# Kernel optimization log

Measured on AMD Instinct MI355X. Metric: run time of the kernel, lower is better.

Reference implementation:

```python
import jax, jax.numpy as jnp
import numpy as np

TAU = 2.0      # LIF membrane time constant (spikingjelly default-style, decay_input=True)
VTH = 0.5      # v_threshold from init
S = 4          # time_steps
EPS = 1e-5     # BatchNorm eps
ALPHA = 4.0    # surrogate sigmoid alpha (spikingjelly Sigmoid default)

@jax.custom_vjp
def spike(x):
    # Heaviside forward (spikingjelly: x >= 0 -> 1)
    return (x >= 0.0).astype(x.dtype)

def _spike_fwd(x):
    return spike(x), x

def _spike_bwd(x, g):
    sg = jax.nn.sigmoid(ALPHA * x)
    return (g * ALPHA * sg * (1.0 - sg),)

spike.defvjp(_spike_fwd, _spike_bwd)

def bn(y, gamma, beta, mean, var):
    # inference-mode BatchNorm2d over channel axis 1; y: (B, C, T, V)
    inv = gamma * jax.lax.rsqrt(var + EPS)
    return y * inv[None, :, None, None] + (beta - mean * inv)[None, :, None, None]


def setup_inputs() -> dict:
    key = jax.random.key(0)
    ks = jax.random.split(key, 16)
    B, T, C, V, H, NC = 16, 512, 3, 16, 128, 12
    inp = {
        "x": jax.random.normal(ks[0], (B, T, C, V), dtype=jnp.float32),
        "w1": jax.random.normal(ks[1], (H, C), dtype=jnp.float32) * (1.0 / np.sqrt(C)),
        "b1": jax.random.normal(ks[2], (H,), dtype=jnp.float32) * 0.01,
        "g1": jnp.ones((H,), jnp.float32),
        "be1": jnp.zeros((H,), jnp.float32),
        "m1": jax.random.normal(ks[3], (H,), dtype=jnp.float32) * 0.1,
        "rv1": jax.random.uniform(ks[4], (H,), dtype=jnp.float32) + 0.5,
        "w2": jax.random.normal(ks[5], (H, H), dtype=jnp.float32) * (1.0 / np.sqrt(H)),
        "b2": jax.random.normal(ks[6], (H,), dtype=jnp.float32) * 0.01,
        "g2": jnp.ones((H,), jnp.float32),
        "be2": jnp.zeros((H,), jnp.float32),
        "m2": jax.random.normal(ks[7], (H,), dtype=jnp.float32) * 0.1,
        "rv2": jax.random.uniform(ks[8], (H,), dtype=jnp.float32) + 0.5,
        "wc": jax.random.normal(ks[9], (NC, H), dtype=jnp.float32) * (1.0 / np.sqrt(H)),
        "bc": jax.random.normal(ks[10], (NC,), dtype=jnp.float32) * 0.01,
    }
    return inp


def reference(x, w1, b1, g1, be1, m1, rv1, w2, b2, g2, be2, m2, rv2, wc, bc):
    # x: (B, T, C, V) -> channels-first (B, C, T, V) as in torch permute
    xc = jnp.transpose(x, (0, 2, 1, 3))
    # fc1 1x1 conv + BN; input identical across all S steps, so compute once
    h1 = bn(jnp.einsum('bctv,oc->botv', xc, w1) + b1[None, :, None, None],
            g1, be1, m1, rv1)  # (B, H, T, V)

    def step(carry, _):
        v1s, v2s, acc = carry
        # LIF1: decay_input=True, v_reset=0 hard reset
        v1n = v1s + (h1 - v1s) / TAU
        s1 = spike(v1n - VTH)
        v1n = v1n * (1.0 - s1)
        # fc2 1x1 conv + BN on spikes
        h2 = bn(jnp.einsum('botv,po->bptv', s1, w2) + b2[None, :, None, None],
                g2, be2, m2, rv2)
        # LIF2
        v2n = v2s + (h2 - v2s) / TAU
        s2 = spike(v2n - VTH)
        v2n = v2n * (1.0 - s2)
        return (v1n, v2n, acc + s2), None

    z = jnp.zeros_like(h1)
    (_, _, acc), _ = jax.lax.scan(step, (z, z, z), None, length=S)
    # mean over S, then mean over T and V -> (B, H); dropout is identity in eval
    feat = (acc / S).mean(axis=(2, 3))
    return feat @ wc.T + bc
```

## Files before the change

kernel.cpp:

```cpp
#include <hip/hip_runtime.h>
#include <stdint.h>
#include <math.h>

#define B_ 16
#define T_ 512
#define C_ 3
#define V_ 16
#define H_ 128
#define NC_ 12

#define WS_W2T   0
#define WS_INV1  16384
#define WS_D1    16512
#define WS_INV2  16640
#define WS_D2    16768
#define WS_FEAT  16896

__global__ void prep_kernel(const float* __restrict__ w2,
                            const float* __restrict__ g1, const float* __restrict__ be1,
                            const float* __restrict__ m1, const float* __restrict__ rv1,
                            const float* __restrict__ g2, const float* __restrict__ be2,
                            const float* __restrict__ m2, const float* __restrict__ rv2,
                            float* __restrict__ ws) {
    int i = blockIdx.x * blockDim.x + threadIdx.x;
    if (i < H_ * H_) {
        int o = i >> 7, p = i & (H_ - 1);
        ws[WS_W2T + i] = w2[p * H_ + o];
    }
    if (i < H_) {
        float r1 = (float)(1.0 / sqrt((double)(rv1[i] + 1e-5f)));
        float inv1 = g1[i] * r1;
        ws[WS_INV1 + i] = inv1;
        ws[WS_D1 + i] = be1[i] - m1[i] * inv1;
        float r2 = (float)(1.0 / sqrt((double)(rv2[i] + 1e-5f)));
        float inv2 = g2[i] * r2;
        ws[WS_INV2 + i] = inv2;
        ws[WS_D2 + i] = be2[i] - m2[i] * inv2;
    }
}

__global__ __launch_bounds__(1024) void snn_main(
    const float* __restrict__ x,
    const float* __restrict__ w1, const float* __restrict__ b1,
    const float* __restrict__ b2, const float* __restrict__ ws,
    float* __restrict__ feat)
{
    __shared__ float smem[H_ * H_];

    const int tid  = threadIdx.x;
    const int lane = tid & 63;
    const int wave = tid >> 6;

    {
        const float4* src = (const float4*)(ws + WS_W2T);
        float4* dst = (float4*)smem;
        #pragma unroll
        for (int i = 0; i < 4; ++i) dst[tid + i * 1024] = src[tid + i * 1024];
    }

    const int p = lane;
    const int q = lane + 64;

    float w10a = w1[p*3+0], w11a = w1[p*3+1], w12a = w1[p*3+2];
    float w10b = w1[q*3+0], w11b = w1[q*3+1], w12b = w1[q*3+2];
    float b1a = b1[p], b1b = b1[q];
    float i1a = ws[WS_INV1+p], i1b = ws[WS_INV1+q];
    float d1a = ws[WS_D1+p],  d1b = ws[WS_D1+q];
    float b2a = b2[p], b2b = b2[q];
    float i2a = ws[WS_INV2+p], i2b = ws[WS_INV2+q];
    float d2a = ws[WS_D2+p],  d2b = ws[WS_D2+q];

    const int b     = blockIdx.x >> 6;
    const int chunk = blockIdx.x & 63;

    float facc_a = 0.f, facc_b = 0.f;

    __syncthreads();

    for (int it = 0; it < 8; ++it) {
        int site = chunk * 128 + it * 16 + wave;
        int t = site >> 4, v = site & 15;
        const float* xp = x + (((size_t)b * T_ + t) * C_) * V_ + v;
        float x0 = xp[0], x1 = xp[V_], x2 = xp[2 * V_];

        float h1a = ((x0 * w10a + x1 * w11a + x2 * w12a) + b1a) * i1a + d1a;
        float h1b = ((x0 * w10b + x1 * w11b + x2 * w12b) + b1b) * i1b + d1b;

        int ka = 0, kb = 0;
        {
            float va = 0.f, vb = 0.f;
            #pragma unroll
            for (int s = 1; s <= 4; ++s) {
                va = va + (h1a - va) * 0.5f;
                vb = vb + (h1b - vb) * 0.5f;
                bool sa  = (va - 0.5f) >= 0.f;
                bool sb2 = (vb - 0.5f) >= 0.f;
                if (sa)  { if (ka == 0) ka = s; va = 0.f; }
                if (sb2) { if (kb == 0) kb = s; vb = 0.f; }
            }
        }

        unsigned long long mA0 = __ballot(ka == 1), mA1 = __ballot(kb == 1);
        unsigned long long mB0 = __ballot(ka == 2), mB1 = __ballot(kb == 2);
        unsigned long long mC0 = __ballot(ka == 3), mC1 = __ballot(kb == 3);
        unsigned long long mD0 = __ballot(ka == 4), mD1 = __ballot(kb == 4);

        float SAa=0,SAb=0,SBa=0,SBb=0,SCa=0,SCb=0,SDa=0,SDb=0;

        #define ACC(mask, obase, Sa, Sb)                            \
            { unsigned long long m = (mask);                        \
              while (m) {                                           \
                  int o = (obase) + __builtin_ctzll(m);             \
                  m &= m - 1;                                       \
                  int idx = o * H_ + p;                             \
                  Sa += smem[idx];                                  \
                  Sb += smem[idx + 64];                             \
              } }

        ACC(mA0, 0, SAa, SAb) ACC(mA1, 64, SAa, SAb)
        ACC(mB0, 0, SBa, SBb) ACC(mB1, 64, SBa, SBb)
        ACC(mC0, 0, SCa, SCb) ACC(mC1, 64, SCa, SCb)
        ACC(mD0, 0, SDa, SDb) ACC(mD1, 64, SDa, SDb)
        #undef ACC

        float r1a = SAa, r2a = SAa + SBa, r3a = SAa + SCa, r4a = SAa + SBa + SDa;
        float r1b = SAb, r2b = SAb + SBb, r3b = SAb + SCb, r4b = SAb + SBb + SDb;

        float h2a[4] = { (r1a + b2a) * i2a + d2a, (r2a + b2a) * i2a + d2a,
                         (r3a + b2a) * i2a + d2a, (r4a + b2a) * i2a + d2a };
        float h2b[4] = { (r1b + b2b) * i2b + d2b, (r2b + b2b) * i2b + d2b,
                         (r3b + b2b) * i2b + d2b, (r4b + b2b) * i2b + d2b };

        float va = 0.f, vb = 0.f;
        #pragma unroll
        for (int s = 0; s < 4; ++s) {
            va = va + (h2a[s] - va) * 0.5f;
            vb = vb + (h2b[s] - vb) * 0.5f;
            bool sa  = (va - 0.5f) >= 0.f;
            bool sb2 = (vb - 0.5f) >= 0.f;
            if (sa)  { facc_a += 1.f; va = 0.f; }
            if (sb2) { facc_b += 1.f; vb = 0.f; }
        }
    }

    __syncthreads();
    smem[wave * H_ + p] = facc_a;
    smem[wave * H_ + q] = facc_b;
    __syncthreads();
    if (wave == 0) {
        float sa = 0.f, sb = 0.f;
        #pragma unroll
        for (int w = 0; w < 16; ++w) { sa += smem[w * H_ + p]; sb += smem[w * H_ + q]; }
        atomicAdd(&feat[b * H_ + p], sa);
        atomicAdd(&feat[b * H_ + q], sb);
    }
}

__global__ void classifier_kernel(const float* __restrict__ feat,
                                  const float* __restrict__ wc,
                                  const float* __restrict__ bc,
                                  float* __restrict__ out) {
    int i = threadIdx.x;
    if (i >= B_ * NC_) return;
    int b = i / NC_, n = i % NC_;
    const float sc = 1.0f / 32768.0f;
    float s = 0.f;
    for (int h = 0; h < H_; ++h) s += (feat[b * H_ + h] * sc) * wc[n * H_ + h];
    out[i] = s + bc[n];
}

extern "C" void kernel_launch(void* const* d_in, const int* in_sizes, int n_in,
                              void* d_out, int out_size, void* d_ws, size_t ws_size,
                              hipStream_t stream) {
    const float* x   = (const float*)d_in[0];
    const float* w1  = (const float*)d_in[1];
    const float* b1  = (const float*)d_in[2];
    const float* g1  = (const float*)d_in[3];
    const float* be1 = (const float*)d_in[4];
    const float* m1  = (const float*)d_in[5];
    const float* rv1 = (const float*)d_in[6];
    const float* w2  = (const float*)d_in[7];
    const float* b2  = (const float*)d_in[8];
    const float* g2  = (const float*)d_in[9];
    const float* be2 = (const float*)d_in[10];
    const float* m2  = (const float*)d_in[11];
    const float* rv2 = (const float*)d_in[12];
    const float* wc  = (const float*)d_in[13];
    const float* bc  = (const float*)d_in[14];
    float* ws  = (float*)d_ws;
    float* out = (float*)d_out;

    prep_kernel<<<64, 256, 0, stream>>>(w2, g1, be1, m1, rv1, g2, be2, m2, rv2, ws);
    hipMemsetAsync(ws + WS_FEAT, 0, B_ * H_ * sizeof(float), stream);
    snn_main<<<1024, 1024, 0, stream>>>(x, w1, b1, b2, ws, ws + WS_FEAT);
    classifier_kernel<<<1, 256, 0, stream>>>(ws + WS_FEAT, wc, bc, out);
}
```

Baseline: 158.6 us.

## Interleave w2 rows for float2 LDS reads, fold memset into prep, parallelize classifier

Reorders the transposed w2 table so each lane's two output channels (p and p+64) sit next to each other, letting the spike-accumulate loop fetch both weights with a single float2 shared-memory load. The memset of the feature accumulator is moved into the prep kernel, removing one stream operation. The classifier now uses one 64-thread block per (batch, class) output with a shuffle reduction instead of a single block doing serial 128-long loops. The float2 access changes the LDS bank pattern, and the prep kernel grows to cover the zeroing range.

```diff
diff --git a/kernel.cpp b/kernel.cpp
--- a/kernel.cpp
+++ b/kernel.cpp
@@ -9,7 +9,7 @@
 #define H_ 128
 #define NC_ 12
 
-#define WS_W2T   0
+#define WS_W2P   0
 #define WS_INV1  16384
 #define WS_D1    16512
 #define WS_INV2  16640
@@ -24,8 +24,11 @@
                             float* __restrict__ ws) {
     int i = blockIdx.x * blockDim.x + threadIdx.x;
     if (i < H_ * H_) {
-        int o = i >> 7, p = i & (H_ - 1);
-        ws[WS_W2T + i] = w2[p * H_ + o];
+        int o = i >> 7, j = i & (H_ - 1);
+        int l = j >> 1, hh = j & 1;
+        ws[WS_W2P + i] = w2[(l + 64 * hh) * H_ + o];
+    } else if (i >= H_ * H_ && i < H_ * H_ + B_ * H_) {
+        ws[WS_FEAT + (i - H_ * H_)] = 0.0f;
     }
     if (i < H_) {
         float r1 = (float)(1.0 / sqrt((double)(rv1[i] + 1e-5f)));
@@ -52,7 +55,7 @@
     const int wave = tid >> 6;
 
     {
-        const float4* src = (const float4*)(ws + WS_W2T);
+        const float4* src = (const float4*)(ws + WS_W2P);
         float4* dst = (float4*)smem;
         #pragma unroll
         for (int i = 0; i < 4; ++i) dst[tid + i * 1024] = src[tid + i * 1024];
@@ -72,6 +75,8 @@
 
     const int b     = blockIdx.x >> 6;
     const int chunk = blockIdx.x & 63;
+
+    const float2* wrow = ((const float2*)smem) + lane;
 
     float facc_a = 0.f, facc_b = 0.f;
 
@@ -112,9 +117,9 @@
               while (m) {                                           \
                   int o = (obase) + __builtin_ctzll(m);             \
                   m &= m - 1;                                       \
-                  int idx = o * H_ + p;                             \
-                  Sa += smem[idx];                                  \
-                  Sb += smem[idx + 64];                             \
+                  float2 wv = wrow[o << 6];                         \
+                  Sa += wv.x;                                       \
+                  Sb += wv.y;                                       \
               } }
 
         ACC(mA0, 0, SAa, SAb) ACC(mA1, 64, SAa, SAb)
@@ -156,17 +161,21 @@
     }
 }
 
-__global__ void classifier_kernel(const float* __restrict__ feat,
-                                  const float* __restrict__ wc,
-                                  const float* __restrict__ bc,
-                                  float* __restrict__ out) {
-    int i = threadIdx.x;
-    if (i >= B_ * NC_) return;
-    int b = i / NC_, n = i % NC_;
+__global__ __launch_bounds__(64) void classifier_kernel(
+    const float* __restrict__ feat,
+    const float* __restrict__ wc,
+    const float* __restrict__ bc,
+    float* __restrict__ out) {
+    int bn = blockIdx.x;
+    int b = bn / NC_, n = bn % NC_;
+    int l = threadIdx.x;
     const float sc = 1.0f / 32768.0f;
-    float s = 0.f;
-    for (int h = 0; h < H_; ++h) s += (feat[b * H_ + h] * sc) * wc[n * H_ + h];
-    out[i] = s + bc[n];
+    float2 f = *(const float2*)(feat + b * H_ + 2 * l);
+    float2 w = *(const float2*)(wc + n * H_ + 2 * l);
+    float s = (f.x * sc) * w.x + (f.y * sc) * w.y;
+    #pragma unroll
+    for (int off = 32; off > 0; off >>= 1) s += __shfl_down(s, off);
+    if (l == 0) out[bn] = s + bc[n];
 }
 
 extern "C" void kernel_launch(void* const* d_in, const int* in_sizes, int n_in,
@@ -190,8 +199,7 @@
     float* ws  = (float*)d_ws;
     float* out = (float*)d_out;
 
-    prep_kernel<<<64, 256, 0, stream>>>(w2, g1, be1, m1, rv1, g2, be2, m2, rv2, ws);
-    hipMemsetAsync(ws + WS_FEAT, 0, B_ * H_ * sizeof(float), stream);
+    prep_kernel<<<80, 256, 0, stream>>>(w2, g1, be1, m1, rv1, g2, be2, m2, rv2, ws);
     snn_main<<<1024, 1024, 0, stream>>>(x, w1, b1, b2, ws, ws + WS_FEAT);
-    classifier_kernel<<<1, 256, 0, stream>>>(ws + WS_FEAT, wc, bc, out);
-}
+    classifier_kernel<<<B_ * NC_, 64, 0, stream>>>(ws + WS_FEAT, wc, bc, out);
+}
```

Result: faster. 147.9 us (-6.7%).

## Compute fc2 spike matmul on MFMA with split-bf16 weights and fused prep

Applied to the files above, without the earlier changes.

Replaces the ballot/ctz sparse gather accumulation of w2 rows with bf16 MFMA 16x16x32 matmuls. Spike masks are expanded to bf16 A fragments via a lookup table, and w2 is split into hi and lo bf16 parts so the result stays close to fp32. The prep kernel is removed: BN folding and the w2 conversion now happen per block, and the classifier is parallelized across batches. This adds redundant per-block weight conversion and extra LDS traffic in exchange for dense matrix throughput.

```diff
diff --git a/kernel.cpp b/kernel.cpp
--- a/kernel.cpp
+++ b/kernel.cpp
@@ -1,172 +1,202 @@
 #include <hip/hip_runtime.h>
+#include <hip/hip_bf16.h>
 #include <stdint.h>
 #include <math.h>
 
 #define B_ 16
 #define T_ 512
-#define C_ 3
 #define V_ 16
 #define H_ 128
 #define NC_ 12
 
-#define WS_W2T   0
-#define WS_INV1  16384
-#define WS_D1    16512
-#define WS_INV2  16640
-#define WS_D2    16768
-#define WS_FEAT  16896
-
-__global__ void prep_kernel(const float* __restrict__ w2,
-                            const float* __restrict__ g1, const float* __restrict__ be1,
-                            const float* __restrict__ m1, const float* __restrict__ rv1,
-                            const float* __restrict__ g2, const float* __restrict__ be2,
-                            const float* __restrict__ m2, const float* __restrict__ rv2,
-                            float* __restrict__ ws) {
-    int i = blockIdx.x * blockDim.x + threadIdx.x;
-    if (i < H_ * H_) {
-        int o = i >> 7, p = i & (H_ - 1);
-        ws[WS_W2T + i] = w2[p * H_ + o];
-    }
-    if (i < H_) {
-        float r1 = (float)(1.0 / sqrt((double)(rv1[i] + 1e-5f)));
-        float inv1 = g1[i] * r1;
-        ws[WS_INV1 + i] = inv1;
-        ws[WS_D1 + i] = be1[i] - m1[i] * inv1;
-        float r2 = (float)(1.0 / sqrt((double)(rv2[i] + 1e-5f)));
-        float inv2 = g2[i] * r2;
-        ws[WS_INV2 + i] = inv2;
-        ws[WS_D2 + i] = be2[i] - m2[i] * inv2;
-    }
-}
-
-__global__ __launch_bounds__(1024) void snn_main(
+typedef float v2f __attribute__((ext_vector_type(2)));
+typedef __attribute__((ext_vector_type(8))) short s8frag;
+typedef __attribute__((ext_vector_type(4))) float f4frag;
+typedef unsigned long long u64;
+
+
+__global__ __launch_bounds__(1024) void zero_feat_kernel(float* __restrict__ feat) {
+    int i = blockIdx.x * 1024 + threadIdx.x;
+    if (i < B_ * H_) feat[i] = 0.f;
+}
+
+__global__ __launch_bounds__(1024, 4) void snn_main(
     const float* __restrict__ x,
     const float* __restrict__ w1, const float* __restrict__ b1,
-    const float* __restrict__ b2, const float* __restrict__ ws,
+    const float* __restrict__ g1, const float* __restrict__ be1,
+    const float* __restrict__ m1, const float* __restrict__ rv1,
+    const float* __restrict__ w2, const float* __restrict__ b2,
+    const float* __restrict__ g2, const float* __restrict__ be2,
+    const float* __restrict__ m2, const float* __restrict__ rv2,
     float* __restrict__ feat)
 {
-    __shared__ float smem[H_ * H_];
+    __shared__ union {
+        unsigned short Bw[2 * H_ * H_];
+        uint4 afrag[16 * 4 * 64];
+    } u;
+    __shared__ u64 mask_lds[64 * 8];
+    __shared__ u64 lut[16];
+    __shared__ float red[8 * 16];
 
     const int tid  = threadIdx.x;
     const int lane = tid & 63;
     const int wave = tid >> 6;
-
-    {
-        const float4* src = (const float4*)(ws + WS_W2T);
-        float4* dst = (float4*)smem;
-        #pragma unroll
-        for (int i = 0; i < 4; ++i) dst[tid + i * 1024] = src[tid + i * 1024];
-    }
-
-    const int p = lane;
-    const int q = lane + 64;
-
-    float w10a = w1[p*3+0], w11a = w1[p*3+1], w12a = w1[p*3+2];
-    float w10b = w1[q*3+0], w11b = w1[q*3+1], w12b = w1[q*3+2];
-    float b1a = b1[p], b1b = b1[q];
-    float i1a = ws[WS_INV1+p], i1b = ws[WS_INV1+q];
-    float d1a = ws[WS_D1+p],  d1b = ws[WS_D1+q];
-    float b2a = b2[p], b2b = b2[q];
-    float i2a = ws[WS_INV2+p], i2b = ws[WS_INV2+q];
-    float d2a = ws[WS_D2+p],  d2b = ws[WS_D2+q];
-
     const int b     = blockIdx.x >> 6;
     const int chunk = blockIdx.x & 63;
-
-    float facc_a = 0.f, facc_b = 0.f;
-
-    __syncthreads();
-
-    for (int it = 0; it < 8; ++it) {
-        int site = chunk * 128 + it * 16 + wave;
-        int t = site >> 4, v = site & 15;
-        const float* xp = x + (((size_t)b * T_ + t) * C_) * V_ + v;
-        float x0 = xp[0], x1 = xp[V_], x2 = xp[2 * V_];
-
-        float h1a = ((x0 * w10a + x1 * w11a + x2 * w12a) + b1a) * i1a + d1a;
-        float h1b = ((x0 * w10b + x1 * w11b + x2 * w12b) + b1b) * i1b + d1b;
-
-        int ka = 0, kb = 0;
-        {
-            float va = 0.f, vb = 0.f;
-            #pragma unroll
-            for (int s = 1; s <= 4; ++s) {
-                va = va + (h1a - va) * 0.5f;
-                vb = vb + (h1b - vb) * 0.5f;
-                bool sa  = (va - 0.5f) >= 0.f;
-                bool sb2 = (vb - 0.5f) >= 0.f;
-                if (sa)  { if (ka == 0) ka = s; va = 0.f; }
-                if (sb2) { if (kb == 0) kb = s; vb = 0.f; }
+    const int slice = wave & 7;
+    const int kg    = lane >> 4;
+
+    if (tid < 16) {
+        u64 v = 0;
+        #pragma unroll
+        for (int j = 0; j < 4; ++j)
+            if ((tid >> j) & 1) v |= (u64)0x3F80u << (16 * j);
+        lut[tid] = v;
+    }
+
+    for (int i = tid; i < H_ * H_; i += 1024) {
+        float w = w2[i];
+        __hip_bfloat16 hb = __float2bfloat16(w);
+        float hf = __bfloat162float(hb);
+        __hip_bfloat16 lb = __float2bfloat16(w - hf);
+        u.Bw[i]            = *(unsigned short*)&hb;
+        u.Bw[H_ * H_ + i]  = *(unsigned short*)&lb;
+    }
+
+    const int p = lane, q = lane + 64;
+    v2f w0v = { w1[p*3+0], w1[q*3+0] };
+    v2f w1v = { w1[p*3+1], w1[q*3+1] };
+    v2f w2v = { w1[p*3+2], w1[q*3+2] };
+    v2f b1v = { b1[p], b1[q] };
+    float i1a = g1[p] * (float)(1.0 / sqrt((double)(rv1[p] + 1e-5f)));
+    float i1b = g1[q] * (float)(1.0 / sqrt((double)(rv1[q] + 1e-5f)));
+    v2f i1v = { i1a, i1b };
+    v2f d1v = { be1[p] - m1[p] * i1a, be1[q] - m1[q] * i1b };
+    const int ch = slice * 16 + (lane & 15);
+    float i2c = g2[ch] * (float)(1.0 / sqrt((double)(rv2[ch] + 1e-5f)));
+    float d2c = be2[ch] - m2[ch] * i2c;
+    float b2c = b2[ch];
+
+    __syncthreads();
+
+    s8frag bhi[4], blo[4];
+    #pragma unroll
+    for (int c = 0; c < 4; ++c) {
+        int idx = ch * H_ + c * 32 + kg * 8;
+        bhi[c] = *(const s8frag*)&u.Bw[idx];
+        blo[c] = *(const s8frag*)&u.Bw[H_ * H_ + idx];
+    }
+    __syncthreads();
+
+    float facc = 0.f;
+    const int tile_own = wave;
+    const int tbase = (wave >> 3) * 8;
+
+    for (int g = 0; g < 2; ++g) {
+        #pragma unroll
+        for (int i = 0; i < 4; ++i) {
+            int sl   = wave + 16 * i;
+            int site = chunk * 128 + g * 64 + sl;
+            int t = site >> 4, v = site & 15;
+            const float* xp = x + ((size_t)(b * T_ + t) * 3) * V_ + v;
+            float x0 = xp[0], x1 = xp[V_], x2 = xp[2 * V_];
+
+            v2f h1 = ((x0 * w0v + x1 * w1v + x2 * w2v) + b1v) * i1v + d1v;
+            v2f v1t = h1 * 0.5f;
+            v2f v2t = v1t + h1 * 0.25f;
+            v2f v3t = v2t + (h1 - v2t) * 0.5f;
+            v2f v4t = v3t + (h1 - v3t) * 0.5f;
+
+            u64 t1a = __ballot(v1t.x >= 0.5f), t2a = __ballot(v2t.x >= 0.5f);
+            u64 t3a = __ballot(v3t.x >= 0.5f), t4a = __ballot(v4t.x >= 0.5f);
+            u64 t1b = __ballot(v1t.y >= 0.5f), t2b = __ballot(v2t.y >= 0.5f);
+            u64 t3b = __ballot(v3t.y >= 0.5f), t4b = __ballot(v4t.y >= 0.5f);
+            u64 s3a = t1a | (t3a & ~t2a), s3b = t1b | (t3b & ~t2b);
+            u64 s4a = t2a | (t4a & ~t3a), s4b = t2b | (t4b & ~t3b);
+
+            if (lane < 8) {
+                int stp = lane >> 1; bool hf = lane & 1;
+                u64 vm;
+                if      (stp == 0) vm = hf ? t1b : t1a;
+                else if (stp == 1) vm = hf ? t2b : t2a;
+                else if (stp == 2) vm = hf ? s3b : s3a;
+                else               vm = hf ? s4b : s4a;
+                mask_lds[sl * 8 + lane] = vm;
             }
         }
-
-        unsigned long long mA0 = __ballot(ka == 1), mA1 = __ballot(kb == 1);
-        unsigned long long mB0 = __ballot(ka == 2), mB1 = __ballot(kb == 2);
-        unsigned long long mC0 = __ballot(ka == 3), mC1 = __ballot(kb == 3);
-        unsigned long long mD0 = __ballot(ka == 4), mD1 = __ballot(kb == 4);
-
-        float SAa=0,SAb=0,SBa=0,SBb=0,SCa=0,SCb=0,SDa=0,SDb=0;
-
-        #define ACC(mask, obase, Sa, Sb)                            \
-            { unsigned long long m = (mask);                        \
-              while (m) {                                           \
-                  int o = (obase) + __builtin_ctzll(m);             \
-                  m &= m - 1;                                       \
-                  int idx = o * H_ + p;                             \
-                  Sa += smem[idx];                                  \
-                  Sb += smem[idx + 64];                             \
-              } }
-
-        ACC(mA0, 0, SAa, SAb) ACC(mA1, 64, SAa, SAb)
-        ACC(mB0, 0, SBa, SBb) ACC(mB1, 64, SBa, SBb)
-        ACC(mC0, 0, SCa, SCb) ACC(mC1, 64, SCa, SCb)
-        ACC(mD0, 0, SDa, SDb) ACC(mD1, 64, SDa, SDb)
-        #undef ACC
-
-        float r1a = SAa, r2a = SAa + SBa, r3a = SAa + SCa, r4a = SAa + SBa + SDa;
-        float r1b = SAb, r2b = SAb + SBb, r3b = SAb + SCb, r4b = SAb + SBb + SDb;
-
-        float h2a[4] = { (r1a + b2a) * i2a + d2a, (r2a + b2a) * i2a + d2a,
-                         (r3a + b2a) * i2a + d2a, (r4a + b2a) * i2a + d2a };
-        float h2b[4] = { (r1b + b2b) * i2b + d2b, (r2b + b2b) * i2b + d2b,
-                         (r3b + b2b) * i2b + d2b, (r4b + b2b) * i2b + d2b };
-
-        float va = 0.f, vb = 0.f;
-        #pragma unroll
-        for (int s = 0; s < 4; ++s) {
-            va = va + (h2a[s] - va) * 0.5f;
-            vb = vb + (h2b[s] - vb) * 0.5f;
-            bool sa  = (va - 0.5f) >= 0.f;
-            bool sb2 = (vb - 0.5f) >= 0.f;
-            if (sa)  { facc_a += 1.f; va = 0.f; }
-            if (sb2) { facc_b += 1.f; vb = 0.f; }
+        __syncthreads();
+
+        {
+            int r   = lane & 15;
+            int sl  = tile_own * 4 + (r >> 2);
+            int stp = r & 3;
+            const unsigned char* mb = (const unsigned char*)&mask_lds[sl * 8 + stp * 2];
+            #pragma unroll
+            for (int c = 0; c < 4; ++c) {
+                unsigned int bt = mb[c * 4 + kg];
+                u64 lo = lut[bt & 15], hi = lut[bt >> 4];
+                uint4 fr;
+                fr.x = (unsigned)lo; fr.y = (unsigned)(lo >> 32);
+                fr.z = (unsigned)hi; fr.w = (unsigned)(hi >> 32);
+                u.afrag[(tile_own * 4 + c) * 64 + lane] = fr;
+            }
         }
-    }
-
-    __syncthreads();
-    smem[wave * H_ + p] = facc_a;
-    smem[wave * H_ + q] = facc_b;
-    __syncthreads();
-    if (wave == 0) {
-        float sa = 0.f, sb = 0.f;
-        #pragma unroll
-        for (int w = 0; w < 16; ++w) { sa += smem[w * H_ + p]; sb += smem[w * H_ + q]; }
-        atomicAdd(&feat[b * H_ + p], sa);
-        atomicAdd(&feat[b * H_ + q], sb);
-    }
-}
-
-__global__ void classifier_kernel(const float* __restrict__ feat,
-                                  const float* __restrict__ wc,
-                                  const float* __restrict__ bc,
-                                  float* __restrict__ out) {
-    int i = threadIdx.x;
-    if (i >= B_ * NC_) return;
-    int b = i / NC_, n = i % NC_;
-    const float sc = 1.0f / 32768.0f;
-    float s = 0.f;
-    for (int h = 0; h < H_; ++h) s += (feat[b * H_ + h] * sc) * wc[n * H_ + h];
-    out[i] = s + bc[n];
+        __syncthreads();
+
+        for (int j = 0; j < 8; ++j) {
+            int tl = tbase + j;
+            s8frag a0 = *(const s8frag*)&u.afrag[(tl * 4 + 0) * 64 + lane];
+            s8frag a1 = *(const s8frag*)&u.afrag[(tl * 4 + 1) * 64 + lane];
+            s8frag a2 = *(const s8frag*)&u.afrag[(tl * 4 + 2) * 64 + lane];
+            s8frag a3 = *(const s8frag*)&u.afrag[(tl * 4 + 3) * 64 + lane];
+            f4frag acc = { 0.f, 0.f, 0.f, 0.f };
+            acc = __builtin_amdgcn_mfma_f32_16x16x32_bf16(a0, bhi[0], acc, 0, 0, 0);
+            acc = __builtin_amdgcn_mfma_f32_16x16x32_bf16(a1, bhi[1], acc, 0, 0, 0);
+            acc = __builtin_amdgcn_mfma_f32_16x16x32_bf16(a2, bhi[2], acc, 0, 0, 0);
+            acc = __builtin_amdgcn_mfma_f32_16x16x32_bf16(a3, bhi[3], acc, 0, 0, 0);
+            acc = __builtin_amdgcn_mfma_f32_16x16x32_bf16(a0, blo[0], acc, 0, 0, 0);
+            acc = __builtin_amdgcn_mfma_f32_16x16x32_bf16(a1, blo[1], acc, 0, 0, 0);
+            acc = __builtin_amdgcn_mfma_f32_16x16x32_bf16(a2, blo[2], acc, 0, 0, 0);
+            acc = __builtin_amdgcn_mfma_f32_16x16x32_bf16(a3, blo[3], acc, 0, 0, 0);
+
+            float vv = 0.f;
+            #pragma unroll
+            for (int s = 0; s < 4; ++s) {
+                float h2 = (acc[s] + b2c) * i2c + d2c;
+                vv = vv + (h2 - vv) * 0.5f;
+                bool sp = vv >= 0.5f;
+                vv = sp ? 0.f : vv;
+                facc += sp ? 1.f : 0.f;
+            }
+        }
+        __syncthreads();
+    }
+
+    facc += __shfl_down(facc, 32);
+    facc += __shfl_down(facc, 16);
+    if (wave < 8) {
+        if (lane < 16) red[slice * 16 + lane] = facc;
+    }
+    __syncthreads();
+    if (wave >= 8 && lane < 16) {
+        atomicAdd(&feat[b * H_ + ch], red[slice * 16 + lane] + facc);
+    }
+}
+
+__global__ __launch_bounds__(128) void classifier_kernel(
+    const float* __restrict__ feat,
+    const float* __restrict__ wc,
+    const float* __restrict__ bc,
+    float* __restrict__ out) {
+    __shared__ float fb[H_];
+    int b = blockIdx.x, t = threadIdx.x;
+    fb[t] = feat[b * H_ + t] * (1.0f / 32768.0f);
+    __syncthreads();
+    if (t < NC_) {
+        float s = 0.f;
+        for (int h = 0; h < H_; ++h) s += fb[h] * wc[t * H_ + h];
+        out[b * NC_ + t] = s + bc[t];
+    }
 }
 
 extern "C" void kernel_launch(void* const* d_in, const int* in_sizes, int n_in,
@@ -187,11 +217,11 @@
     const float* rv2 = (const float*)d_in[12];
     const float* wc  = (const float*)d_in[13];
     const float* bc  = (const float*)d_in[14];
-    float* ws  = (float*)d_ws;
-    float* out = (float*)d_out;
-
-    prep_kernel<<<64, 256, 0, stream>>>(w2, g1, be1, m1, rv1, g2, be2, m2, rv2, ws);
-    hipMemsetAsync(ws + WS_FEAT, 0, B_ * H_ * sizeof(float), stream);
-    snn_main<<<1024, 1024, 0, stream>>>(x, w1, b1, b2, ws, ws + WS_FEAT);
-    classifier_kernel<<<1, 256, 0, stream>>>(ws + WS_FEAT, wc, bc, out);
-}
+    float* feat = (float*)d_ws;
+    float* out  = (float*)d_out;
+
+    zero_feat_kernel<<<2, 1024, 0, stream>>>(feat);
+    snn_main<<<1024, 1024, 0, stream>>>(x, w1, b1, g1, be1, m1, rv1,
+                                        w2, b2, g2, be2, m2, rv2, feat);
+    classifier_kernel<<<B_, 128, 0, stream>>>(feat, wc, bc, out);
+}
```

Result: faster. 154.9 us (-2.3%).
